# Kernel tuning notes

Measured on AMD Instinct MI355X. Metric: run time of the kernel, lower is better.

## Reference

```python
import jax, jax.numpy as jnp
import numpy as np

L = 3
ALPHA = 1.0
BETA = 1.0
SCALING = 3.0
N_NODES = 100000
N_EDGES = 1250000
D_FEAT = 64


def spmm(row, col, w, z, n):
    # out[i] = sum_{e: row_e == i} w_e * z[col_e]  (torch_sparse.matmul reduce='sum')
    return jax.ops.segment_sum(z[col] * w[:, None], row, num_segments=n)


def setup_inputs() -> dict:
    key = jax.random.key(0)
    k1, k2, k3, k4 = jax.random.split(key, 4)
    x = jax.random.normal(k1, (N_NODES, D_FEAT), dtype=jnp.float32)
    edge_index = jax.random.randint(k2, (2, N_EDGES), 0, N_NODES, dtype=jnp.int64)
    # surrogate for symmetric-normalized adjacency weights
    edge_weight = jax.random.uniform(k3, (N_EDGES,), dtype=jnp.float32) * 0.2
    gammas = jnp.full((L + 1, 1), min(1.0 / SCALING, 1.0), dtype=jnp.float32)
    return {"x": x, "edge_index": edge_index, "edge_weight": edge_weight, "gammas": gammas}


def reference(x, edge_index, edge_weight, gammas):
    n = x.shape[0]
    row, col = edge_index[0], edge_index[1]
    a, b = ALPHA, BETA

    zs = [x]  # z_0 = x
    # l = 1: c * z0 + (a+b+2)/2 * A z0
    z1 = ((a - b) / 2) * zs[-1] + ((a + b + 2) / 2) * spmm(row, col, edge_weight, zs[-1], n)
    zs.append(z1)
    for l in range(2, L + 1):
        c0 = 2 * l * (l + a + b) * (2 * l + a + b - 2)
        c1 = (2 * l + a + b - 1) * (a ** 2 - b ** 2)
        c2 = (2 * l + a + b - 1) * (2 * l + a + b) * (2 * l + a + b - 2)
        c3 = 2 * (l + a - 1) * (l + b - 1) * (2 * l + a + b)
        Az = spmm(row, col, edge_weight, zs[-1], n)
        z = (c1 * zs[-1] + c2 * Az - c3 * zs[-2]) / c0
        zs.append(z)

    coefs = jnp.cumprod(jnp.tanh(gammas) * SCALING, axis=0)  # [L+1, 1]
    Z = jnp.stack(zs, axis=1)  # [N, L+1, d]
    return (Z * coefs).mean(axis=1)
```

## Files before the change

### kernel.cpp

```cpp
#include <hip/hip_runtime.h>
#include <hip/hip_fp16.h>
#include <math.h>

#define D 64
#define RB_SHIFT 7
#define RB 128
#define CAP 2048
#define CAPE 3072
#define MAX_NB 1024


__global__ void bin_scatter_kernel(const int* __restrict__ row, const int* __restrict__ col,
                                   const float* __restrict__ w,
                                   int* __restrict__ cursor,
                                   int2* __restrict__ binned, int E, int NB) {
    __shared__ int lbase[MAX_NB];
    __shared__ int lcur[MAX_NB];
    int chunk = (E + gridDim.x - 1) / gridDim.x;
    int lo = blockIdx.x * chunk;
    int hi = min(E, lo + chunk);
    for (int j = threadIdx.x; j < NB; j += blockDim.x) { lbase[j] = 0; lcur[j] = 0; }
    __syncthreads();
    for (int i = lo + threadIdx.x; i < hi; i += blockDim.x)
        atomicAdd(&lbase[row[i] >> RB_SHIFT], 1);
    __syncthreads();
    for (int j = threadIdx.x; j < NB; j += blockDim.x) {
        int c = lbase[j];
        int base = c ? atomicAdd(&cursor[j], c) : 0;
        lbase[j] = j * CAP + base;
    }
    __syncthreads();
    for (int i = lo + threadIdx.x; i < hi; i += blockDim.x) {
        int r = row[i];
        int b = r >> RB_SHIFT;
        int off = atomicAdd(&lcur[b], 1);
        binned[lbase[b] + off] = make_int2(col[i] | ((r & (RB - 1)) << 17), __float_as_int(w[i]));
    }
}

__global__ void bucket_sort_kernel(const int2* __restrict__ binned,
                                   const int* __restrict__ cursor,
                                   int2* __restrict__ edges, int2* __restrict__ rowinfo,
                                   int N, int NB) {
    __shared__ int2 elds[CAP];
    __shared__ int2 perm[CAPE];
    __shared__ int hist[RB];
    __shared__ int scn[RB];
    __shared__ int pst[RB];
    __shared__ int cur[RB];
    int b = blockIdx.x, t = threadIdx.x;
    int base = b * CAP;
    int cnt = cursor[b];
    if (cnt > CAP) cnt = CAP;

    for (int i = t; i < cnt; i += 256) elds[i] = binned[base + i];
    if (t < RB) hist[t] = 0;
    __syncthreads();
    for (int i = t; i < cnt; i += 256) atomicAdd(&hist[(elds[i].x >> 17) & (RB - 1)], 1);
    __syncthreads();
    if (t < RB) scn[t] = (hist[t] + 7) & ~7;
    __syncthreads();
    for (int off = 1; off < RB; off <<= 1) {
        int v = (t < RB && t >= off) ? scn[t - off] : 0;
        __syncthreads();
        if (t < RB) scn[t] += v;
        __syncthreads();
    }
    if (t < RB) {
        int pl = (hist[t] + 7) & ~7;
        int ps = scn[t] - pl;
        pst[t] = ps;
        cur[t] = ps;
    }
    __syncthreads();
    for (int i = t; i < cnt; i += 256) {
        int rl = (elds[i].x >> 17) & (RB - 1);
        int d = atomicAdd(&cur[rl], 1);
        perm[d] = make_int2(elds[i].x & 0x1FFFF, elds[i].y);
    }
    __syncthreads();
    if (t < RB) {
        int h = hist[t];
        int ps = pst[t];
        int pl = (h + 7) & ~7;
        int dummycol = (h > 0) ? perm[ps].x : 0;
        for (int i = h; i < pl; ++i) perm[ps + i] = make_int2(dummycol, 0);
        int r0 = b * RB + t;
        if (r0 < N) rowinfo[r0] = make_int2(b * CAPE + ps, pl);
    }
    __syncthreads();
    int ptotal = scn[RB - 1];
    for (int i = t; i < ptotal; i += 256) edges[b * CAPE + i] = perm[i];
}

__global__ void tohalf_kernel(const float4* __restrict__ in, ushort4* __restrict__ o, int n4) {
    int i = blockIdx.x * blockDim.x + threadIdx.x;
    int stride = gridDim.x * blockDim.x;
    for (; i < n4; i += stride) {
        float4 f = in[i];
        ushort4 h;
        h.x = __half_as_ushort(__float2half(f.x));
        h.y = __half_as_ushort(__float2half(f.y));
        h.z = __half_as_ushort(__float2half(f.z));
        h.w = __half_as_ushort(__float2half(f.w));
        o[i] = h;
    }
}

__device__ __forceinline__ float2 row_gather_acc2(const int2* __restrict__ ep, int cnt,
                                                  const __half2* __restrict__ g2, int lane) {
    int k = lane & 31;
    bool up = (lane >> 5) != 0;
    float2 acc = make_float2(0.f, 0.f);
    for (int jb = 0; jb < cnt; jb += 8) {
        int2 ed[8];
#pragma unroll
        for (int q = 0; q < 8; ++q) ed[q] = ep[jb + q];
        float2 v[4];
#pragma unroll
        for (int q = 0; q < 4; ++q) {
            int c0 = __builtin_amdgcn_readfirstlane(ed[2 * q].x);
            int c1 = __builtin_amdgcn_readfirstlane(ed[2 * q + 1].x);
            int c  = up ? c1 : c0;
            v[q] = __half22float2(g2[(size_t)c * 32 + k]);
        }
#pragma unroll
        for (int q = 0; q < 4; ++q) {
            float w0 = __int_as_float(__builtin_amdgcn_readfirstlane(ed[2 * q].y));
            float w1 = __int_as_float(__builtin_amdgcn_readfirstlane(ed[2 * q + 1].y));
            float wt = up ? w1 : w0;
            acc.x = fmaf(wt, v[q].x, acc.x);
            acc.y = fmaf(wt, v[q].y, acc.y);
        }
    }
    acc.x += __shfl_xor(acc.x, 32, 64);
    acc.y += __shfl_xor(acc.y, 32, 64);
    return acc;
}

__global__ void spmm_z_kernel(const int2* __restrict__ rowinfo,
                              const int2* __restrict__ edges,
                              const __half2* __restrict__ gsrc2,
                              const __half2* __restrict__ zp2_2,
                              __half2* __restrict__ zdst2,
                              float cA, float cC, int N) {
    int gid = blockIdx.x * blockDim.x + threadIdx.x;
    int r = gid >> 6;
    int lane = threadIdx.x & 63;
    if (r >= N) return;

    int2 ri = rowinfo[r];
    int k0  = __builtin_amdgcn_readfirstlane(ri.x);
    int cnt = __builtin_amdgcn_readfirstlane(ri.y);

    float2 acc = row_gather_acc2(edges + k0, cnt, gsrc2, lane);

    if ((lane >> 5) == 0) {
        int k = lane & 31;
        size_t idx2 = (size_t)r * 32 + k;
        float2 z = make_float2(cA * acc.x, cA * acc.y);
        if (zp2_2) {
            float2 p2 = __half22float2(zp2_2[idx2]);
            z.x = fmaf(cC, p2.x, z.x);
            z.y = fmaf(cC, p2.y, z.y);
        }
        zdst2[idx2] = __floats2half2_rn(z.x, z.y);
    }
}

__global__ void spmm_final_kernel(const int2* __restrict__ rowinfo,
                                  const int2* __restrict__ edges,
                                  const __half2* __restrict__ z2h2,
                                  const __half2* __restrict__ z1h2,
                                  const __half2* __restrict__ xh2,
                                  float* __restrict__ out,
                                  const float* __restrict__ gammas,
                                  float cA, float cC, int N) {
    int gid = blockIdx.x * blockDim.x + threadIdx.x;
    int r = gid >> 6;
    int lane = threadIdx.x & 63;
    if (r >= N) return;

    float t0 = tanhf(gammas[0]) * 3.0f;
    float t1 = t0 * (tanhf(gammas[1]) * 3.0f);
    float t2 = t1 * (tanhf(gammas[2]) * 3.0f);
    float t3 = t2 * (tanhf(gammas[3]) * 3.0f);

    int2 ri = rowinfo[r];
    int k0  = __builtin_amdgcn_readfirstlane(ri.x);
    int cnt = __builtin_amdgcn_readfirstlane(ri.y);

    float2 acc = row_gather_acc2(edges + k0, cnt, z2h2, lane);

    if ((lane >> 5) == 0) {
        int k = lane & 31;
        size_t idx2 = (size_t)r * 32 + k;
        float2 z1v = __half22float2(z1h2[idx2]);
        float2 z2v = __half22float2(z2h2[idx2]);
        float2 xv  = __half22float2(xh2[idx2]);
        float2 z3 = make_float2(cA * acc.x + cC * z1v.x, cA * acc.y + cC * z1v.y);
        float2 o;
        o.x = 0.25f * (t0 * xv.x + t1 * z1v.x + t2 * z2v.x + t3 * z3.x);
        o.y = 0.25f * (t0 * xv.y + t1 * z1v.y + t2 * z2v.y + t3 * z3.y);
        ((float2*)out)[idx2] = o;
    }
}

extern "C" void kernel_launch(void* const* d_in, const int* in_sizes, int n_in,
                              void* d_out, int out_size, void* d_ws, size_t ws_size,
                              hipStream_t stream) {
    const float* x      = (const float*)d_in[0];
    const int*   ei     = (const int*)d_in[1];
    const float* w      = (const float*)d_in[2];
    const float* gammas = (const float*)d_in[3];

    const int E = in_sizes[1] / 2;
    const int N = in_sizes[0] / D;
    const long NF = (long)N * D;
    const int NB = (N + RB - 1) >> RB_SHIFT;

    float* out = (float*)d_out;

    char* p = (char*)d_ws;
    __half* xh  = (__half*)p;       p += NF * sizeof(__half);
    __half* z1h = (__half*)p;       p += NF * sizeof(__half);
    __half* z2h = (__half*)p;       p += NF * sizeof(__half);
    int* cursor = (int*)p;          p += NB * sizeof(int);
    p = (char*)(((uintptr_t)p + 15) & ~(uintptr_t)15);
    int2* rowinfo = (int2*)p;       p += (size_t)N * sizeof(int2);
    int2* binned = (int2*)p;        p += (size_t)NB * CAP * sizeof(int2);
    int2* edges = (int2*)p;

    const int* row = ei;
    const int* col = ei + E;

    const double a = 1.0, b = 1.0;
    const int blk = 256;

    hipMemsetAsync(cursor, 0, (size_t)NB * sizeof(int), stream);
    bin_scatter_kernel<<<256, 1024, 0, stream>>>(row, col, w, cursor, binned, E, NB);
    bucket_sort_kernel<<<NB, 256, 0, stream>>>(binned, cursor, edges, rowinfo, N, NB);
    tohalf_kernel<<<1024, blk, 0, stream>>>((const float4*)x, (ushort4*)xh, (int)(NF / 4));

    const int sgrid = (N + 3) / 4;

    {
        float cA = (float)((a + b + 2.0) / 2.0);
        spmm_z_kernel<<<sgrid, blk, 0, stream>>>(rowinfo, edges, (const __half2*)xh,
                                                 nullptr, (__half2*)z1h, cA, 0.0f, N);
    }

    {
        int l = 2;
        double c0 = 2.0 * l * (l + a + b) * (2.0 * l + a + b - 2.0);
        double c2 = (2.0 * l + a + b - 1.0) * (2.0 * l + a + b) * (2.0 * l + a + b - 2.0);
        double c3 = 2.0 * (l + a - 1.0) * (l + b - 1.0) * (2.0 * l + a + b);
        spmm_z_kernel<<<sgrid, blk, 0, stream>>>(rowinfo, edges, (const __half2*)z1h,
                                                 (const __half2*)xh, (__half2*)z2h,
                                                 (float)(c2 / c0), (float)(-c3 / c0), N);
    }

    {
        int l = 3;
        double c0 = 2.0 * l * (l + a + b) * (2.0 * l + a + b - 2.0);
        double c2 = (2.0 * l + a + b - 1.0) * (2.0 * l + a + b) * (2.0 * l + a + b - 2.0);
        double c3 = 2.0 * (l + a - 1.0) * (l + b - 1.0) * (2.0 * l + a + b);
        spmm_final_kernel<<<sgrid, blk, 0, stream>>>(rowinfo, edges, (const __half2*)z2h,
                                                     (const __half2*)z1h, (const __half2*)xh,
                                                     out, gammas,
                                                     (float)(c2 / c0), (float)(-c3 / c0), N);
    }
}
```

Before: 238.6 us.

## Process two rows per wavefront with packed-half FMA and prescaled edge columns

Each wavefront now handles two rows, one per 32-lane half, instead of splitting one row's edges across halves and reducing with a shuffle. Rows are padded pairwise to the same length so the loop count stays wavefront-uniform. Edge weights are stored as duplicated half2 and column indices are prescaled into byte offsets, so the inner loop does a raw gather and a packed __hfma2. Bins shrink to 64 rows with a direct global-read bucket sort instead of an LDS copy. Accumulating in fp16 cuts ALU and register work but adds rounding error, and pairwise padding adds some dummy edges.

```diff
diff --git a/kernel.cpp b/kernel.cpp
--- a/kernel.cpp
+++ b/kernel.cpp
@@ -3,11 +3,11 @@
 #include <math.h>
 
 #define D 64
-#define RB_SHIFT 7
-#define RB 128
-#define CAP 2048
-#define CAPE 3072
-#define MAX_NB 1024
+#define RB_SHIFT 6
+#define RB 64
+#define CAP 1024
+#define CAPE 2048
+#define MAX_NB 1600
 
 
 __global__ void bin_scatter_kernel(const int* __restrict__ row, const int* __restrict__ col,
@@ -42,9 +42,9 @@
                                    const int* __restrict__ cursor,
                                    int2* __restrict__ edges, int2* __restrict__ rowinfo,
                                    int N, int NB) {
-    __shared__ int2 elds[CAP];
     __shared__ int2 perm[CAPE];
     __shared__ int hist[RB];
+    __shared__ int plr[RB];
     __shared__ int scn[RB];
     __shared__ int pst[RB];
     __shared__ int cur[RB];
@@ -53,12 +53,14 @@
     int cnt = cursor[b];
     if (cnt > CAP) cnt = CAP;
 
-    for (int i = t; i < cnt; i += 256) elds[i] = binned[base + i];
     if (t < RB) hist[t] = 0;
     __syncthreads();
-    for (int i = t; i < cnt; i += 256) atomicAdd(&hist[(elds[i].x >> 17) & (RB - 1)], 1);
-    __syncthreads();
-    if (t < RB) scn[t] = (hist[t] + 7) & ~7;
+    for (int i = t; i < cnt; i += 256)
+        atomicAdd(&hist[(binned[base + i].x >> 17) & (RB - 1)], 1);
+    __syncthreads();
+    if (t < RB) plr[t] = (hist[t] + 7) & ~7;
+    __syncthreads();
+    if (t < RB) scn[t] = max(plr[t], plr[t ^ 1]);
     __syncthreads();
     for (int off = 1; off < RB; off <<= 1) {
         int v = (t < RB && t >= off) ? scn[t - off] : 0;
@@ -67,22 +69,24 @@
         __syncthreads();
     }
     if (t < RB) {
-        int pl = (hist[t] + 7) & ~7;
+        int pl = max(plr[t], plr[t ^ 1]);
         int ps = scn[t] - pl;
         pst[t] = ps;
         cur[t] = ps;
     }
     __syncthreads();
     for (int i = t; i < cnt; i += 256) {
-        int rl = (elds[i].x >> 17) & (RB - 1);
+        int2 e = binned[base + i];
+        int rl = (e.x >> 17) & (RB - 1);
         int d = atomicAdd(&cur[rl], 1);
-        perm[d] = make_int2(elds[i].x & 0x1FFFF, elds[i].y);
+        __half2 wh2 = __half2half2(__float2half(__int_as_float(e.y)));
+        perm[d] = make_int2((e.x & 0x1FFFF) << 7, *(int*)&wh2);
     }
     __syncthreads();
     if (t < RB) {
         int h = hist[t];
         int ps = pst[t];
-        int pl = (h + 7) & ~7;
+        int pl = max(plr[t], plr[t ^ 1]);
         int dummycol = (h > 0) ? perm[ps].x : 0;
         for (int i = h; i < pl; ++i) perm[ps + i] = make_int2(dummycol, 0);
         int r0 = b * RB + t;
@@ -90,6 +94,7 @@
     }
     __syncthreads();
     int ptotal = scn[RB - 1];
+    if (ptotal > CAPE) ptotal = CAPE;
     for (int i = t; i < ptotal; i += 256) edges[b * CAPE + i] = perm[i];
 }
 
@@ -107,34 +112,23 @@
     }
 }
 
-__device__ __forceinline__ float2 row_gather_acc2(const int2* __restrict__ ep, int cnt,
-                                                  const __half2* __restrict__ g2, int lane) {
-    int k = lane & 31;
-    bool up = (lane >> 5) != 0;
-    float2 acc = make_float2(0.f, 0.f);
+__device__ __forceinline__ __half2 half_row_acc(const int2* __restrict__ ep, int cnt,
+                                                const char* __restrict__ g2b, int koff) {
+    __half2 acc = __half2half2(__ushort_as_half((unsigned short)0));
     for (int jb = 0; jb < cnt; jb += 8) {
-        int2 ed[8];
+        int2 dd[8];
 #pragma unroll
-        for (int q = 0; q < 8; ++q) ed[q] = ep[jb + q];
-        float2 v[4];
+        for (int q = 0; q < 8; ++q) dd[q] = ep[jb + q];
+        __half2 v[8];
 #pragma unroll
-        for (int q = 0; q < 4; ++q) {
-            int c0 = __builtin_amdgcn_readfirstlane(ed[2 * q].x);
-            int c1 = __builtin_amdgcn_readfirstlane(ed[2 * q + 1].x);
-            int c  = up ? c1 : c0;
-            v[q] = __half22float2(g2[(size_t)c * 32 + k]);
+        for (int q = 0; q < 8; ++q)
+            v[q] = *(const __half2*)(g2b + (size_t)(unsigned)(dd[q].x + koff));
+#pragma unroll
+        for (int q = 0; q < 8; ++q) {
+            int wb = dd[q].y;
+            acc = __hfma2(*(__half2*)&wb, v[q], acc);
         }
-#pragma unroll
-        for (int q = 0; q < 4; ++q) {
-            float w0 = __int_as_float(__builtin_amdgcn_readfirstlane(ed[2 * q].y));
-            float w1 = __int_as_float(__builtin_amdgcn_readfirstlane(ed[2 * q + 1].y));
-            float wt = up ? w1 : w0;
-            acc.x = fmaf(wt, v[q].x, acc.x);
-            acc.y = fmaf(wt, v[q].y, acc.y);
-        }
-    }
-    acc.x += __shfl_xor(acc.x, 32, 64);
-    acc.y += __shfl_xor(acc.y, 32, 64);
+    }
     return acc;
 }
 
@@ -145,27 +139,28 @@
                               __half2* __restrict__ zdst2,
                               float cA, float cC, int N) {
     int gid = blockIdx.x * blockDim.x + threadIdx.x;
-    int r = gid >> 6;
+    int wv = gid >> 6;
     int lane = threadIdx.x & 63;
-    if (r >= N) return;
+    int half = lane >> 5;
+    int k = lane & 31;
+    int r = 2 * wv + half;
+    if (2 * wv >= N) return;
+    if (r >= N) r = N - 1;
 
     int2 ri = rowinfo[r];
-    int k0  = __builtin_amdgcn_readfirstlane(ri.x);
     int cnt = __builtin_amdgcn_readfirstlane(ri.y);
 
-    float2 acc = row_gather_acc2(edges + k0, cnt, gsrc2, lane);
-
-    if ((lane >> 5) == 0) {
-        int k = lane & 31;
-        size_t idx2 = (size_t)r * 32 + k;
-        float2 z = make_float2(cA * acc.x, cA * acc.y);
-        if (zp2_2) {
-            float2 p2 = __half22float2(zp2_2[idx2]);
-            z.x = fmaf(cC, p2.x, z.x);
-            z.y = fmaf(cC, p2.y, z.y);
-        }
-        zdst2[idx2] = __floats2half2_rn(z.x, z.y);
-    }
+    __half2 acc = half_row_acc(edges + ri.x, cnt, (const char*)gsrc2, k * 4);
+    float2 a = __half22float2(acc);
+
+    size_t idx2 = (size_t)r * 32 + k;
+    float2 z = make_float2(cA * a.x, cA * a.y);
+    if (zp2_2) {
+        float2 p2 = __half22float2(zp2_2[idx2]);
+        z.x = fmaf(cC, p2.x, z.x);
+        z.y = fmaf(cC, p2.y, z.y);
+    }
+    zdst2[idx2] = __floats2half2_rn(z.x, z.y);
 }
 
 __global__ void spmm_final_kernel(const int2* __restrict__ rowinfo,
@@ -177,9 +172,13 @@
                                   const float* __restrict__ gammas,
                                   float cA, float cC, int N) {
     int gid = blockIdx.x * blockDim.x + threadIdx.x;
-    int r = gid >> 6;
+    int wv = gid >> 6;
     int lane = threadIdx.x & 63;
-    if (r >= N) return;
+    int half = lane >> 5;
+    int k = lane & 31;
+    int r = 2 * wv + half;
+    if (2 * wv >= N) return;
+    if (r >= N) r = N - 1;
 
     float t0 = tanhf(gammas[0]) * 3.0f;
     float t1 = t0 * (tanhf(gammas[1]) * 3.0f);
@@ -187,23 +186,20 @@
     float t3 = t2 * (tanhf(gammas[3]) * 3.0f);
 
     int2 ri = rowinfo[r];
-    int k0  = __builtin_amdgcn_readfirstlane(ri.x);
     int cnt = __builtin_amdgcn_readfirstlane(ri.y);
 
-    float2 acc = row_gather_acc2(edges + k0, cnt, z2h2, lane);
-
-    if ((lane >> 5) == 0) {
-        int k = lane & 31;
-        size_t idx2 = (size_t)r * 32 + k;
-        float2 z1v = __half22float2(z1h2[idx2]);
-        float2 z2v = __half22float2(z2h2[idx2]);
-        float2 xv  = __half22float2(xh2[idx2]);
-        float2 z3 = make_float2(cA * acc.x + cC * z1v.x, cA * acc.y + cC * z1v.y);
-        float2 o;
-        o.x = 0.25f * (t0 * xv.x + t1 * z1v.x + t2 * z2v.x + t3 * z3.x);
-        o.y = 0.25f * (t0 * xv.y + t1 * z1v.y + t2 * z2v.y + t3 * z3.y);
-        ((float2*)out)[idx2] = o;
-    }
+    __half2 acc = half_row_acc(edges + ri.x, cnt, (const char*)z2h2, k * 4);
+    float2 a = __half22float2(acc);
+
+    size_t idx2 = (size_t)r * 32 + k;
+    float2 z1v = __half22float2(z1h2[idx2]);
+    float2 z2v = __half22float2(z2h2[idx2]);
+    float2 xv  = __half22float2(xh2[idx2]);
+    float2 z3 = make_float2(cA * a.x + cC * z1v.x, cA * a.y + cC * z1v.y);
+    float2 o;
+    o.x = 0.25f * (t0 * xv.x + t1 * z1v.x + t2 * z2v.x + t3 * z3.x);
+    o.y = 0.25f * (t0 * xv.y + t1 * z1v.y + t2 * z2v.y + t3 * z3.y);
+    ((float2*)out)[idx2] = o;
 }
 
 extern "C" void kernel_launch(void* const* d_in, const int* in_sizes, int n_in,
@@ -242,7 +238,8 @@
     bucket_sort_kernel<<<NB, 256, 0, stream>>>(binned, cursor, edges, rowinfo, N, NB);
     tohalf_kernel<<<1024, blk, 0, stream>>>((const float4*)x, (ushort4*)xh, (int)(NF / 4));
 
-    const int sgrid = (N + 3) / 4;
+    const int nwaves = (N + 1) / 2;
+    const int sgrid = (nwaves + 3) / 4;
 
     {
         float cA = (float)((a + b + 2.0) / 2.0);
```

New measurement: 206.6 us. -13.4%, faster.
